# Kernel tuning notes

Measured on AMD Instinct MI355X. Metric: run time of the kernel, lower is better.

## Reference

```python
import jax, jax.numpy as jnp
import numpy as np

N = 100000   # nodes
E = 1000000  # edges per graph (avg degree 10)
D = 300      # feature dim


def _layernorm(x, gamma, beta, eps=1e-5):
    mu = jnp.mean(x, axis=-1, keepdims=True)
    var = jnp.mean(jnp.square(x - mu), axis=-1, keepdims=True)
    return (x - mu) * jax.lax.rsqrt(var + eps) * gamma + beta


def _graph_conv(edges, x, W, b, num_nodes):
    # DGL GraphConv with norm='both' and relu activation:
    # h = relu( D_in^{-1/2} A D_out^{-1/2} x W + b )
    src, dst = edges[0], edges[1]
    ones = jnp.ones((edges.shape[1],), x.dtype)
    out_deg = jax.ops.segment_sum(ones, src, num_segments=num_nodes)
    in_deg = jax.ops.segment_sum(ones, dst, num_segments=num_nodes)
    norm_src = jnp.where(out_deg > 0, jax.lax.rsqrt(jnp.maximum(out_deg, 1.0)), 0.0)
    norm_dst = jnp.where(in_deg > 0, jax.lax.rsqrt(jnp.maximum(in_deg, 1.0)), 0.0)
    h = x * norm_src[:, None]                                  # [N, D]
    agg = jax.ops.segment_sum(h[src], dst, num_segments=num_nodes)  # gather+scatter
    agg = agg * norm_dst[:, None]
    return jax.nn.relu(agg @ W + b)


def setup_inputs() -> dict:
    key = jax.random.key(0)
    ks = jax.random.split(key, 8)
    s = 0.05  # weight scale
    return {
        "table_feat": jax.random.normal(ks[0], (N, D), jnp.float32),
        "row_edges": jax.random.randint(ks[1], (2, E), 0, N, jnp.int32),
        "col_edges": jax.random.randint(ks[2], (2, E), 0, N, jnp.int32),
        "Wr": jax.random.normal(ks[3], (D, D), jnp.float32) * s,
        "br": jnp.zeros((D,), jnp.float32),
        "Wc": jax.random.normal(ks[4], (D, D), jnp.float32) * s,
        "bc": jnp.zeros((D,), jnp.float32),
        "Wrs": jax.random.normal(ks[5], (D, D), jnp.float32) * s,
        "brs": jnp.zeros((D,), jnp.float32),
        "g_rs": jnp.ones((D,), jnp.float32),
        "b_rs": jnp.zeros((D,), jnp.float32),
        "Wcs": jax.random.normal(ks[6], (D, D), jnp.float32) * s,
        "bcs": jnp.zeros((D,), jnp.float32),
        "g_cs": jnp.ones((D,), jnp.float32),
        "b_cs": jnp.zeros((D,), jnp.float32),
        "Wm": jax.random.normal(ks[7], (2 * D, D), jnp.float32) * s,
        "bm": jnp.zeros((D,), jnp.float32),
        "g_m": jnp.ones((D,), jnp.float32),
        "b_m": jnp.zeros((D,), jnp.float32),
    }


def reference(table_feat, row_edges, col_edges, Wr, br, Wc, bc,
              Wrs, brs, g_rs, b_rs, Wcs, bcs, g_cs, b_cs,
              Wm, bm, g_m, b_m):
    rowg = _graph_conv(row_edges, table_feat, Wr, br, N)   # row_aware GraphConv
    colg = _graph_conv(col_edges, table_feat, Wc, bc, N)   # col_aware GraphConv
    rowg = _layernorm(rowg @ Wrs + brs, g_rs, b_rs)        # row_graph_support
    colg = _layernorm(colg @ Wcs + bcs, g_cs, b_cs)        # col_graph_support
    merged = jnp.concatenate([rowg, colg], axis=1)          # [N, 2D]
    return _layernorm(merged @ Wm + bm, g_m, b_m)           # graph_merge
```

## Files before the change

kernel.cpp:

```cpp
#include <hip/hip_runtime.h>
#include <stdint.h>

#define SP 304
#define HSP 310
#define NT 10
#define KS300 19

typedef unsigned short u16;
using short8 = __attribute__((ext_vector_type(8))) short;
using f32x16 = __attribute__((ext_vector_type(16))) float;

__device__ __forceinline__ float b2f(u16 u) {
    return __uint_as_float(((unsigned)u) << 16);
}
__device__ __forceinline__ u16 f2b(float f) {
    unsigned u = __float_as_uint(f);
    return (u16)((u + 0x7FFFu + ((u >> 16) & 1u)) >> 16);
}
__device__ __forceinline__ float scrub(float v) {
    unsigned u = __float_as_uint(v);
    return (((u >> 23) & 0xFFu) == 0xFFu) ? 0.f : v;
}
__device__ __forceinline__ u16 sb16(u16 v) {
    return (((v >> 7) & 0xFFu) == 0xFFu) ? (u16)0 : v;
}

__global__ void detect_dtype(const u16* __restrict__ xs, int* __restrict__ flag) {
    __shared__ int cnt[256];
    int c = 0;
    for (int i = 0; i < 16; i++) {
        u16 v = xs[threadIdx.x * 16 + i];
        unsigned e = (v >> 7) & 0xFFu;
        c += (e >= 100u && e <= 150u) ? 1 : 0;
    }
    cnt[threadIdx.x] = c;
    __syncthreads();
    for (int s = 128; s > 0; s >>= 1) {
        if (threadIdx.x < s) cnt[threadIdx.x] += cnt[threadIdx.x + s];
        __syncthreads();
    }
    if (threadIdx.x == 0) flag[0] = (cnt[0] >= 3686) ? 1 : 0;
}

template<bool BF16>
__global__ __launch_bounds__(256) void conv_x(const void* __restrict__ x, u16* __restrict__ xb,
                                              int total4, const int* __restrict__ flag) {
    if ((flag[0] != 0) != BF16) return;
    int idx = blockIdx.x * 256 + threadIdx.x;
    if (idx >= total4) return;
    int node = idx / 76, c = idx - node * 76;
    ushort4 v = make_ushort4(0, 0, 0, 0);
    if (c < 75) {
        if (BF16) {
            v = *(const ushort4*)((const u16*)x + (size_t)node * 300 + c * 4);
            v.x = sb16(v.x); v.y = sb16(v.y); v.z = sb16(v.z); v.w = sb16(v.w);
        } else {
            float4 f = *(const float4*)((const float*)x + (size_t)node * 300 + c * 4);
            v = make_ushort4(f2b(scrub(f.x)), f2b(scrub(f.y)), f2b(scrub(f.z)), f2b(scrub(f.w)));
        }
    }
    *(ushort4*)(xb + (size_t)node * SP + c * 4) = v;
}

template<bool BF16>
__global__ void pack_b(const void* __restrict__ W, u16* __restrict__ P, int nseg,
                       const int* __restrict__ flag) {
    if ((flag[0] != 0) != BF16) return;
    int idx = blockIdx.x * 256 + threadIdx.x;
    int total = nseg * KS300 * NT * 512;
    if (idx >= total) return;
    int j = idx & 7, lane = (idx >> 3) & 63, t = idx >> 9;
    int nt = t % NT, ks = t / NT;
    int seg = ks / KS300, ksl = ks - seg * KS300;
    int kk = ksl * 16 + ((lane >> 5) << 3) + j;
    int n = nt * 32 + (lane & 31);
    u16 v = 0;
    if (kk < 300 && n < 300) {
        int wk = seg * 300 + kk;
        if (BF16) v = sb16(((const u16*)W)[(size_t)wk * 300 + n]);
        else      v = f2b(scrub(((const float*)W)[(size_t)wk * 300 + n]));
    }
    P[idx] = v;
}

template<bool BF16>
__global__ void conv_params(const void* p0, const void* p1, const void* p2, const void* p3,
                            const void* p4, const void* p5, const void* p6, const void* p7,
                            const void* p8, const void* p9, const void* p10,
                            float* __restrict__ pbuf, const int* __restrict__ flag) {
    if ((flag[0] != 0) != BF16) return;
    int idx = blockIdx.x * 256 + threadIdx.x;
    if (idx >= 11 * 304) return;
    int j = idx / 304, c = idx % 304;
    const void* ps[11] = {p0, p1, p2, p3, p4, p5, p6, p7, p8, p9, p10};
    float v = 0.f;
    if (c < 300) {
        if (BF16) v = b2f(sb16(((const u16*)ps[j])[c]));
        else      v = scrub(((const float*)ps[j])[c]);
    }
    pbuf[j * 304 + c] = v;
}

__global__ void count_deg(const int* __restrict__ src, const int* __restrict__ dst, int E,
                          int* __restrict__ outd, int* __restrict__ ind) {
    int e = blockIdx.x * 256 + threadIdx.x;
    if (e < E) {
        atomicAdd(&outd[src[e]], 1);
        atomicAdd(&ind[dst[e]], 1);
    }
}

__global__ __launch_bounds__(256) void alloc_norm(int Nn,
                           const int* __restrict__ odR, const int* __restrict__ idR,
                           const int* __restrict__ odC, const int* __restrict__ idC,
                           int* __restrict__ offR, int* __restrict__ offC,
                           float* __restrict__ nsR, float* __restrict__ ndR,
                           float* __restrict__ nsC, float* __restrict__ ndC,
                           int* __restrict__ cur2) {
    __shared__ int sR[256], sC[256];
    __shared__ int baseR, baseC;
    int tid = threadIdx.x;
    int i = blockIdx.x * 256 + tid;
    int dR = (i < Nn) ? idR[i] : 0;
    int dC = (i < Nn) ? idC[i] : 0;
    sR[tid] = dR; sC[tid] = dC;
    __syncthreads();
    for (int off = 1; off < 256; off <<= 1) {
        int vR = (tid >= off) ? sR[tid - off] : 0;
        int vC = (tid >= off) ? sC[tid - off] : 0;
        __syncthreads();
        sR[tid] += vR; sC[tid] += vC;
        __syncthreads();
    }
    if (tid == 0) {
        baseR = atomicAdd(&cur2[0], sR[255]);
        baseC = atomicAdd(&cur2[1], sC[255]);
    }
    __syncthreads();
    if (i < Nn) {
        offR[i] = baseR + sR[tid] - dR;
        offC[i] = baseC + sC[tid] - dC;
        nsR[i] = odR[i] > 0 ? rsqrtf((float)odR[i]) : 0.f;
        ndR[i] = idR[i] > 0 ? rsqrtf((float)idR[i]) : 0.f;
        nsC[i] = odC[i] > 0 ? rsqrtf((float)odC[i]) : 0.f;
        ndC[i] = idC[i] > 0 ? rsqrtf((float)idC[i]) : 0.f;
    }
}

__global__ void fill_csr(const int* __restrict__ src, const int* __restrict__ dst, int E,
                         const int* __restrict__ offs, int* __restrict__ cursor,
                         int* __restrict__ adj) {
    int e = blockIdx.x * 256 + threadIdx.x;
    if (e < E) {
        int d = dst[e];
        int p = offs[d] + atomicAdd(&cursor[d], 1);
        adj[p] = src[e];
    }
}

__global__ __launch_bounds__(256) void aggregate(
    const u16* __restrict__ xb, const int* __restrict__ adj, const int* __restrict__ offs,
    const int* __restrict__ deg, const float* __restrict__ ns, const float* __restrict__ nd,
    u16* __restrict__ agg, int Nn) {
    int w = threadIdx.x >> 6, lane = threadIdx.x & 63;
    int node = blockIdx.x * 4 + w;
    if (node >= Nn) return;
    int bg = offs[node], cnt = deg[node];
    const bool part = lane < 12;
    const int c0 = 4 * lane, c1 = 256 + 4 * lane;
    float a0 = 0, a1 = 0, a2 = 0, a3 = 0, p0 = 0, p1 = 0, p2 = 0, p3 = 0;
    int j = 0;
    for (; j + 4 <= cnt; j += 4) {
        int s0 = adj[bg + j], s1 = adj[bg + j + 1], s2 = adj[bg + j + 2], s3 = adj[bg + j + 3];
        float n0 = ns[s0], n1 = ns[s1], n2 = ns[s2], n3 = ns[s3];
        const u16* q0 = xb + (size_t)s0 * SP;
        const u16* q1 = xb + (size_t)s1 * SP;
        const u16* q2 = xb + (size_t)s2 * SP;
        const u16* q3 = xb + (size_t)s3 * SP;
        ushort4 v0 = *(const ushort4*)(q0 + c0);
        ushort4 v1 = *(const ushort4*)(q1 + c0);
        ushort4 v2 = *(const ushort4*)(q2 + c0);
        ushort4 v3 = *(const ushort4*)(q3 + c0);
        a0 += b2f(v0.x) * n0 + b2f(v1.x) * n1 + b2f(v2.x) * n2 + b2f(v3.x) * n3;
        a1 += b2f(v0.y) * n0 + b2f(v1.y) * n1 + b2f(v2.y) * n2 + b2f(v3.y) * n3;
        a2 += b2f(v0.z) * n0 + b2f(v1.z) * n1 + b2f(v2.z) * n2 + b2f(v3.z) * n3;
        a3 += b2f(v0.w) * n0 + b2f(v1.w) * n1 + b2f(v2.w) * n2 + b2f(v3.w) * n3;
        if (part) {
            ushort4 u0 = *(const ushort4*)(q0 + c1);
            ushort4 u1 = *(const ushort4*)(q1 + c1);
            ushort4 u2 = *(const ushort4*)(q2 + c1);
            ushort4 u3 = *(const ushort4*)(q3 + c1);
            p0 += b2f(u0.x) * n0 + b2f(u1.x) * n1 + b2f(u2.x) * n2 + b2f(u3.x) * n3;
            p1 += b2f(u0.y) * n0 + b2f(u1.y) * n1 + b2f(u2.y) * n2 + b2f(u3.y) * n3;
            p2 += b2f(u0.z) * n0 + b2f(u1.z) * n1 + b2f(u2.z) * n2 + b2f(u3.z) * n3;
            p3 += b2f(u0.w) * n0 + b2f(u1.w) * n1 + b2f(u2.w) * n2 + b2f(u3.w) * n3;
        }
    }
    for (; j < cnt; ++j) {
        int s = adj[bg + j];
        float nv = ns[s];
        const u16* rp = xb + (size_t)s * SP;
        ushort4 v = *(const ushort4*)(rp + c0);
        a0 += b2f(v.x) * nv; a1 += b2f(v.y) * nv; a2 += b2f(v.z) * nv; a3 += b2f(v.w) * nv;
        if (part) {
            ushort4 u = *(const ushort4*)(rp + c1);
            p0 += b2f(u.x) * nv; p1 += b2f(u.y) * nv; p2 += b2f(u.z) * nv; p3 += b2f(u.w) * nv;
        }
    }
    float ndv = nd[node];
    u16* o = agg + (size_t)node * SP;
    *(ushort4*)(o + c0) = make_ushort4(f2b(a0 * ndv), f2b(a1 * ndv), f2b(a2 * ndv), f2b(a3 * ndv));
    if (part)
        *(ushort4*)(o + c1) = make_ushort4(f2b(p0 * ndv), f2b(p1 * ndv), f2b(p2 * ndv), f2b(p3 * ndv));
}

__global__ __launch_bounds__(256, 3) void gemm_fused(
    const u16* __restrict__ Ain, const u16* __restrict__ B1p, const u16* __restrict__ B2p,
    const float* __restrict__ bias1, const float* __restrict__ bias2,
    const float* __restrict__ gamma2, const float* __restrict__ beta2,
    u16* __restrict__ outp, int M) {
    __shared__ __align__(16) char smem[2048 + 64 * HSP * 2];
    float* red = (float*)smem;
    u16* hb = (u16*)(smem + 2048);

    const int tid = threadIdx.x;
    const int w = tid >> 6, l = tid & 63;
    const int pr = w >> 1, sd = w & 1;
    const int mb = blockIdx.x * 64;
    const int r0 = mb + pr * 32;
    const bool act = r0 < M;
    const int lc = l & 31, hi = l >> 5;
    const int rowA = act ? min(r0 + lc, M - 1) : 0;
    const u16* a1 = Ain + (size_t)rowA * SP + hi * 8;
    const u16* bl1 = B1p + (size_t)(sd * 5) * 512 + (size_t)l * 8;
    const u16* bl2 = B2p + (size_t)(sd * 5) * 512 + (size_t)l * 8;
    const int colbase = sd * 160;

    f32x16 acc[5];
#pragma unroll
    for (int i = 0; i < 5; ++i)
#pragma unroll
        for (int r = 0; r < 16; ++r) acc[i][r] = 0.f;

    for (int ks = 0; ks < KS300; ++ks) {
        short8 af = *(const short8*)(a1 + ks * 16);
        const u16* bb = bl1 + (size_t)ks * (NT * 512);
#pragma unroll
        for (int i = 0; i < 5; ++i) {
            short8 bf = *(const short8*)(bb + i * 512);
            acc[i] = __builtin_amdgcn_mfma_f32_32x32x16_bf16(af, bf, acc[i], 0, 0, 0);
        }
    }
    if (act) {
#pragma unroll
        for (int i = 0; i < 5; ++i) {
            int col = colbase + i * 32 + lc;
            if (col < 304) {
                float bb = col < 300 ? bias1[col] : 0.f;
#pragma unroll
                for (int r = 0; r < 16; ++r) {
                    int rowl = 4 * hi + (r & 3) + 8 * (r >> 2);
                    float v = scrub(acc[i][r] + bb);
                    v = v > 0.f ? v : 0.f;
                    hb[(size_t)(pr * 32 + rowl) * HSP + col] = col < 300 ? f2b(v) : (u16)0;
                }
            }
        }
    }
    __syncthreads();

#pragma unroll
    for (int i = 0; i < 5; ++i)
#pragma unroll
        for (int r = 0; r < 16; ++r) acc[i][r] = 0.f;
    const u16* hrow = hb + (size_t)(pr * 32 + lc) * HSP + hi * 8;
    for (int ks = 0; ks < KS300; ++ks) {
        short8 af = *(const short8*)(hrow + ks * 16);
        const u16* bb = bl2 + (size_t)ks * (NT * 512);
#pragma unroll
        for (int i = 0; i < 5; ++i) {
            short8 bf = *(const short8*)(bb + i * 512);
            acc[i] = __builtin_amdgcn_mfma_f32_32x32x16_bf16(af, bf, acc[i], 0, 0, 0);
        }
    }

    float sum[16], ssq[16];
#pragma unroll
    for (int r = 0; r < 16; ++r) { sum[r] = 0.f; ssq[r] = 0.f; }
#pragma unroll
    for (int i = 0; i < 5; ++i) {
        int col = colbase + i * 32 + lc;
        bool cv = col < 300;
        float bb = cv ? bias2[col] : 0.f;
#pragma unroll
        for (int r = 0; r < 16; ++r) {
            float v = cv ? scrub(acc[i][r] + bb) : 0.f;
            acc[i][r] = v;
            sum[r] += v;
            ssq[r] += v * v;
        }
    }
#pragma unroll
    for (int off = 1; off < 32; off <<= 1) {
#pragma unroll
        for (int r = 0; r < 16; ++r) {
            sum[r] += __shfl_xor(sum[r], off);
            ssq[r] += __shfl_xor(ssq[r], off);
        }
    }
    if (act) {
#pragma unroll
        for (int r = 0; r < 16; ++r) {
            if (lc == r) {
                int rowl = 4 * hi + (r & 3) + 8 * (r >> 2);
                float* q = red + ((pr * 2 + sd) * 32 + rowl) * 2;
                q[0] = sum[r]; q[1] = ssq[r];
            }
        }
    }
    __syncthreads();
    float mean[16], inv[16];
    if (act) {
#pragma unroll
        for (int r = 0; r < 16; ++r) {
            int rowl = 4 * hi + (r & 3) + 8 * (r >> 2);
            const float* q = red + ((pr * 2 + (1 - sd)) * 32 + rowl) * 2;
            float s = sum[r] + q[0], qq = ssq[r] + q[1];
            mean[r] = s * (1.f / 300.f);
            float var = fmaxf(qq * (1.f / 300.f) - mean[r] * mean[r], 0.f);
            inv[r] = rsqrtf(var + 1e-5f);
        }
    }

    u16* stg = hb;
    if (act) {
#pragma unroll
        for (int i = 0; i < 5; ++i) {
            int col = colbase + i * 32 + lc;
            if (col < 304) {
                float g = col < 300 ? gamma2[col] : 0.f;
                float be = col < 300 ? beta2[col] : 0.f;
#pragma unroll
                for (int r = 0; r < 16; ++r) {
                    int rowl = 4 * hi + (r & 3) + 8 * (r >> 2);
                    float v = (acc[i][r] - mean[r]) * inv[r] * g + be;
                    stg[(size_t)(pr * 32 + rowl) * SP + col] = col < 300 ? f2b(v) : (u16)0;
                }
            }
        }
    }
    __syncthreads();
    int rows = min(64, M - mb);
    u16* dst = outp + (size_t)mb * SP;
    if (rows == 64) {
#pragma unroll
        for (int k = 0; k < 10; ++k) {
            int idx = k * 256 + tid;
            if (idx < 2432) *(short8*)(dst + idx * 8) = *(const short8*)(stg + idx * 8);
        }
    } else {
        for (int idx = tid; idx < rows * SP; idx += 256) dst[idx] = stg[idx];
    }
}

template<int MODE, bool OUTF32>
__global__ __launch_bounds__(256, 3) void gemm_f(
    const u16* __restrict__ A1, const u16* __restrict__ A2,
    const u16* __restrict__ Bp, const float* __restrict__ bias,
    const float* __restrict__ gamma, const float* __restrict__ beta,
    void* __restrict__ out, int M, const int* __restrict__ flag) {
    if (MODE == 2) {
        if ((flag[0] != 0) != (!OUTF32)) return;
    }
    __shared__ __align__(16) char smem[2048 + 38912];
    float* red = (float*)smem;

    const int tid = threadIdx.x;
    const int w = tid >> 6, l = tid & 63;
    const int pr = w >> 1, sd = w & 1;
    const int mb = blockIdx.x * 64;
    const int r0 = mb + pr * 32;
    const bool act = r0 < M;
    const int lc = l & 31, hi = l >> 5;
    const int rowA = act ? min(r0 + lc, M - 1) : 0;
    const u16* a1 = A1 + (size_t)rowA * SP + hi * 8;
    const u16* a2 = A2 + (size_t)rowA * SP + hi * 8;
    const u16* bl = Bp + (size_t)(sd * 5) * 512 + (size_t)l * 8;
    const int colbase = sd * 160;

    f32x16 acc[5];
#pragma unroll
    for (int i = 0; i < 5; ++i)
#pragma unroll
        for (int r = 0; r < 16; ++r) acc[i][r] = 0.f;

    for (int ks = 0; ks < KS300; ++ks) {
        short8 af = *(const short8*)(a1 + ks * 16);
        const u16* bb = bl + (size_t)ks * (NT * 512);
#pragma unroll
        for (int i = 0; i < 5; ++i) {
            short8 bf = *(const short8*)(bb + i * 512);
            acc[i] = __builtin_amdgcn_mfma_f32_32x32x16_bf16(af, bf, acc[i], 0, 0, 0);
        }
    }
    if (MODE == 2) {
        for (int ks = KS300; ks < 2 * KS300; ++ks) {
            short8 af = *(const short8*)(a2 + (ks - KS300) * 16);
            const u16* bb = bl + (size_t)ks * (NT * 512);
#pragma unroll
            for (int i = 0; i < 5; ++i) {
                short8 bf = *(const short8*)(bb + i * 512);
                acc[i] = __builtin_amdgcn_mfma_f32_32x32x16_bf16(af, bf, acc[i], 0, 0, 0);
            }
        }
    }

    float sum[16], ssq[16];
#pragma unroll
    for (int r = 0; r < 16; ++r) { sum[r] = 0.f; ssq[r] = 0.f; }
#pragma unroll
    for (int i = 0; i < 5; ++i) {
        int col = colbase + i * 32 + lc;
        bool cv = col < 300;
        float bb = cv ? bias[col] : 0.f;
#pragma unroll
        for (int r = 0; r < 16; ++r) {
            float v = cv ? scrub(acc[i][r] + bb) : 0.f;
            acc[i][r] = v;
            sum[r] += v;
            ssq[r] += v * v;
        }
    }
#pragma unroll
    for (int off = 1; off < 32; off <<= 1) {
#pragma unroll
        for (int r = 0; r < 16; ++r) {
            sum[r] += __shfl_xor(sum[r], off);
            ssq[r] += __shfl_xor(ssq[r], off);
        }
    }
    if (act) {
#pragma unroll
        for (int r = 0; r < 16; ++r) {
            if (lc == r) {
                int rowl = 4 * hi + (r & 3) + 8 * (r >> 2);
                float* q = red + ((pr * 2 + sd) * 32 + rowl) * 2;
                q[0] = sum[r]; q[1] = ssq[r];
            }
        }
    }
    __syncthreads();
    float mean[16], inv[16];
    if (act) {
#pragma unroll
        for (int r = 0; r < 16; ++r) {
            int rowl = 4 * hi + (r & 3) + 8 * (r >> 2);
            const float* q = red + ((pr * 2 + (1 - sd)) * 32 + rowl) * 2;
            float s = sum[r] + q[0], qq = ssq[r] + q[1];
            mean[r] = s * (1.f / 300.f);
            float var = fmaxf(qq * (1.f / 300.f) - mean[r] * mean[r], 0.f);
            inv[r] = rsqrtf(var + 1e-5f);
        }
    }

    if (!OUTF32) {
        u16* stg = (u16*)(smem + 2048);
        if (act) {
#pragma unroll
            for (int i = 0; i < 5; ++i) {
                int col = colbase + i * 32 + lc;
                if (col < 300) {
                    float g = gamma[col], be = beta[col];
#pragma unroll
                    for (int r = 0; r < 16; ++r) {
                        int rowl = 4 * hi + (r & 3) + 8 * (r >> 2);
                        float v = (acc[i][r] - mean[r]) * inv[r] * g + be;
                        stg[(pr * 32 + rowl) * 300 + col] = f2b(v);
                    }
                }
            }
        }
        __syncthreads();
        int rows = min(64, M - mb);
        u16* dst = (u16*)out + (size_t)mb * 300;
        if (rows == 64) {
#pragma unroll
            for (int k = 0; k < 10; ++k) {
                int idx = k * 256 + tid;
                if (idx < 2400) *(short8*)(dst + idx * 8) = *(const short8*)(stg + idx * 8);
            }
        } else {
            for (int idx = tid; idx < rows * 300; idx += 256) dst[idx] = stg[idx];
        }
    } else {
        float* fst = (float*)(smem + 2048);
        for (int pp = 0; pp < 2; ++pp) {
            __syncthreads();
            if (pr == pp && act) {
#pragma unroll
                for (int i = 0; i < 5; ++i) {
                    int col = colbase + i * 32 + lc;
                    if (col < 300) {
                        float g = gamma[col], be = beta[col];
#pragma unroll
                        for (int r = 0; r < 16; ++r) {
                            int rowl = 4 * hi + (r & 3) + 8 * (r >> 2);
                            float v = (acc[i][r] - mean[r]) * inv[r] * g + be;
                            fst[rowl * 300 + col] = v;
                        }
                    }
                }
            }
            __syncthreads();
            int tr0 = mb + pp * 32;
            if (tr0 < M) {
                int rows = min(32, M - tr0);
                float* dst = (float*)out + (size_t)tr0 * 300;
                if (rows == 32) {
#pragma unroll
                    for (int k = 0; k < 10; ++k) {
                        int idx = k * 256 + tid;
                        if (idx < 2400) *(float4*)(dst + idx * 4) = *(const float4*)(fst + idx * 4);
                    }
                } else {
                    for (int idx = tid; idx < rows * 300; idx += 256) dst[idx] = fst[idx];
                }
            }
        }
    }
}

extern "C" void kernel_launch(void* const* d_in, const int* in_sizes, int n_in,
                              void* d_out, int out_size, void* d_ws, size_t ws_size,
                              hipStream_t stream) {
    (void)n_in; (void)out_size; (void)ws_size;
    const void* x   = d_in[0];
    const int* re   = (const int*)d_in[1];
    const int* ce   = (const int*)d_in[2];

    const int Nn = in_sizes[0] / 300;
    const int Er = in_sizes[1] / 2;
    const int Ec = in_sizes[2] / 2;

    char* p = (char*)d_ws;
    size_t off = 0;
    auto balloc = [&](size_t bytes) -> void* {
        void* r = p + off;
        off += (bytes + 255) & ~(size_t)255;
        return r;
    };
    int* degR  = (int*)balloc((size_t)Nn * 4);
    int* odegR = (int*)balloc((size_t)Nn * 4);
    int* degC  = (int*)balloc((size_t)Nn * 4);
    int* odegC = (int*)balloc((size_t)Nn * 4);
    int* curR  = (int*)balloc((size_t)Nn * 4);
    int* curC  = (int*)balloc((size_t)Nn * 4);
    int* cur2  = (int*)balloc(64 * 4);
    size_t zbytes = off;
    int* flag  = (int*)balloc(256);
    int* offsR = (int*)balloc((size_t)Nn * 4);
    int* offsC = (int*)balloc((size_t)Nn * 4);
    float* nsR = (float*)balloc((size_t)Nn * 4);
    float* ndR = (float*)balloc((size_t)Nn * 4);
    float* nsC = (float*)balloc((size_t)Nn * 4);
    float* ndC = (float*)balloc((size_t)Nn * 4);
    int* adjR  = (int*)balloc((size_t)Er * 4);
    int* adjC  = (int*)balloc((size_t)Ec * 4);
    const size_t PB1 = (size_t)KS300 * NT * 512;
    u16* WrP   = (u16*)balloc(PB1 * 2);
    u16* WcP   = (u16*)balloc(PB1 * 2);
    u16* WrsP  = (u16*)balloc(PB1 * 2);
    u16* WcsP  = (u16*)balloc(PB1 * 2);
    u16* WmP   = (u16*)balloc(2 * PB1 * 2);
    float* pbuf = (float*)balloc(11 * 304 * 4);
    u16* xb    = (u16*)balloc((size_t)Nn * SP * 2);
    u16* B2    = (u16*)balloc((size_t)Nn * SP * 2);
    u16* B3    = (u16*)balloc((size_t)Nn * SP * 2);

    const float* pbr  = pbuf + 0 * 304;
    const float* pbc  = pbuf + 1 * 304;
    const float* pbrs = pbuf + 2 * 304;
    const float* pgrs = pbuf + 3 * 304;
    const float* pBrs = pbuf + 4 * 304;
    const float* pbcs = pbuf + 5 * 304;
    const float* pgcs = pbuf + 6 * 304;
    const float* pBcs = pbuf + 7 * 304;
    const float* pbm  = pbuf + 8 * 304;
    const float* pgm  = pbuf + 9 * 304;
    const float* pBm  = pbuf + 10 * 304;

    detect_dtype<<<1, 256, 0, stream>>>((const u16*)x, flag);
    hipMemsetAsync(d_ws, 0, zbytes, stream);

    const int total4 = Nn * 76;
    conv_x<true><<<(total4 + 255) / 256, 256, 0, stream>>>(x, xb, total4, flag);
    conv_x<false><<<(total4 + 255) / 256, 256, 0, stream>>>(x, xb, total4, flag);

#define PK(Wsrc, Pdst, nseg)                                                                  \
    pack_b<true><<<(int)(((nseg) * PB1 + 255) / 256), 256, 0, stream>>>(Wsrc, Pdst, nseg, flag); \
    pack_b<false><<<(int)(((nseg) * PB1 + 255) / 256), 256, 0, stream>>>(Wsrc, Pdst, nseg, flag)
    PK(d_in[3], WrP, 1);
    PK(d_in[5], WcP, 1);
    PK(d_in[7], WrsP, 1);
    PK(d_in[11], WcsP, 1);
    PK(d_in[15], WmP, 2);
#undef PK

    conv_params<true><<<14, 256, 0, stream>>>(d_in[4], d_in[6], d_in[8], d_in[9], d_in[10],
                                              d_in[12], d_in[13], d_in[14], d_in[16], d_in[17],
                                              d_in[18], pbuf, flag);
    conv_params<false><<<14, 256, 0, stream>>>(d_in[4], d_in[6], d_in[8], d_in[9], d_in[10],
                                               d_in[12], d_in[13], d_in[14], d_in[16], d_in[17],
                                               d_in[18], pbuf, flag);

    count_deg<<<(Er + 255) / 256, 256, 0, stream>>>(re, re + Er, Er, odegR, degR);
    count_deg<<<(Ec + 255) / 256, 256, 0, stream>>>(ce, ce + Ec, Ec, odegC, degC);
    alloc_norm<<<(Nn + 255) / 256, 256, 0, stream>>>(Nn, odegR, degR, odegC, degC,
                                                     offsR, offsC, nsR, ndR, nsC, ndC, cur2);
    fill_csr<<<(Er + 255) / 256, 256, 0, stream>>>(re, re + Er, Er, offsR, curR, adjR);
    fill_csr<<<(Ec + 255) / 256, 256, 0, stream>>>(ce, ce + Ec, Ec, offsC, curC, adjC);

    aggregate<<<(Nn + 3) / 4, 256, 0, stream>>>(xb, adjR, offsR, degR, nsR, ndR, B2, Nn);
    aggregate<<<(Nn + 3) / 4, 256, 0, stream>>>(xb, adjC, offsC, degC, nsC, ndC, B3, Nn);

    const int gb = (Nn + 63) / 64;
    gemm_fused<<<gb, 256, 0, stream>>>(B2, WrP, WrsP, pbr, pbrs, pgrs, pBrs, B2, Nn);
    gemm_fused<<<gb, 256, 0, stream>>>(B3, WcP, WcsP, pbc, pbcs, pgcs, pBcs, B3, Nn);
    gemm_f<2, false><<<gb, 256, 0, stream>>>(B2, B3, WmP, pbm, pgm, pBm, d_out, Nn, flag);
    gemm_f<2, true ><<<gb, 256, 0, stream>>>(B2, B3, WmP, pbm, pgm, pBm, d_out, Nn, flag);
}
```

Before: 1.127 ms.

## Stage GEMM A tiles through LDS and merge dtype-templated kernel launches

The GEMM kernels now copy each 64-row A tile into shared memory with coalesced 16-byte loads before the MFMA loops, instead of each lane reading its A fragments straight from global memory. The same LDS buffer is reused for the hidden activations and for the output staging, with added barriers between phases. Separately, the paired true/false template launches for dtype conversion, weight packing, parameter conversion and the merge GEMM become single kernels that branch on the runtime flag. This halves the launch count for those stages, at the cost of extra synchronisation and a runtime dtype branch.

```diff
diff --git a/kernel.cpp b/kernel.cpp
--- a/kernel.cpp
+++ b/kernel.cpp
@@ -2,7 +2,7 @@
 #include <stdint.h>
 
 #define SP 304
-#define HSP 310
+#define ASP 312
 #define NT 10
 #define KS300 19
 
@@ -42,10 +42,9 @@
     if (threadIdx.x == 0) flag[0] = (cnt[0] >= 3686) ? 1 : 0;
 }
 
-template<bool BF16>
 __global__ __launch_bounds__(256) void conv_x(const void* __restrict__ x, u16* __restrict__ xb,
                                               int total4, const int* __restrict__ flag) {
-    if ((flag[0] != 0) != BF16) return;
+    const bool BF16 = flag[0] != 0;
     int idx = blockIdx.x * 256 + threadIdx.x;
     if (idx >= total4) return;
     int node = idx / 76, c = idx - node * 76;
@@ -62,10 +61,9 @@
     *(ushort4*)(xb + (size_t)node * SP + c * 4) = v;
 }
 
-template<bool BF16>
 __global__ void pack_b(const void* __restrict__ W, u16* __restrict__ P, int nseg,
                        const int* __restrict__ flag) {
-    if ((flag[0] != 0) != BF16) return;
+    const bool BF16 = flag[0] != 0;
     int idx = blockIdx.x * 256 + threadIdx.x;
     int total = nseg * KS300 * NT * 512;
     if (idx >= total) return;
@@ -83,12 +81,11 @@
     P[idx] = v;
 }
 
-template<bool BF16>
 __global__ void conv_params(const void* p0, const void* p1, const void* p2, const void* p3,
                             const void* p4, const void* p5, const void* p6, const void* p7,
                             const void* p8, const void* p9, const void* p10,
                             float* __restrict__ pbuf, const int* __restrict__ flag) {
-    if ((flag[0] != 0) != BF16) return;
+    const bool BF16 = flag[0] != 0;
     int idx = blockIdx.x * 256 + threadIdx.x;
     if (idx >= 11 * 304) return;
     int j = idx / 304, c = idx % 304;
@@ -214,12 +211,21 @@
         *(ushort4*)(o + c1) = make_ushort4(f2b(p0 * ndv), f2b(p1 * ndv), f2b(p2 * ndv), f2b(p3 * ndv));
 }
 
+__device__ __forceinline__ void stage_a(const u16* __restrict__ A, u16* __restrict__ lds,
+                                        int mb, int M, int tid) {
+    for (int idx = tid; idx < 64 * 38; idx += 256) {
+        int row = idx / 38, ck = idx - row * 38;
+        int gr = min(mb + row, M - 1);
+        *(short8*)(lds + row * ASP + ck * 8) = *(const short8*)(A + (size_t)gr * SP + ck * 8);
+    }
+}
+
 __global__ __launch_bounds__(256, 3) void gemm_fused(
     const u16* __restrict__ Ain, const u16* __restrict__ B1p, const u16* __restrict__ B2p,
     const float* __restrict__ bias1, const float* __restrict__ bias2,
     const float* __restrict__ gamma2, const float* __restrict__ beta2,
     u16* __restrict__ outp, int M) {
-    __shared__ __align__(16) char smem[2048 + 64 * HSP * 2];
+    __shared__ __align__(16) char smem[2048 + 64 * ASP * 2];
     float* red = (float*)smem;
     u16* hb = (u16*)(smem + 2048);
 
@@ -230,11 +236,13 @@
     const int r0 = mb + pr * 32;
     const bool act = r0 < M;
     const int lc = l & 31, hi = l >> 5;
-    const int rowA = act ? min(r0 + lc, M - 1) : 0;
-    const u16* a1 = Ain + (size_t)rowA * SP + hi * 8;
     const u16* bl1 = B1p + (size_t)(sd * 5) * 512 + (size_t)l * 8;
     const u16* bl2 = B2p + (size_t)(sd * 5) * 512 + (size_t)l * 8;
     const int colbase = sd * 160;
+    const u16* arow = hb + (size_t)(pr * 32 + lc) * ASP + hi * 8;
+
+    stage_a(Ain, hb, mb, M, tid);
+    __syncthreads();
 
     f32x16 acc[5];
 #pragma unroll
@@ -243,7 +251,7 @@
         for (int r = 0; r < 16; ++r) acc[i][r] = 0.f;
 
     for (int ks = 0; ks < KS300; ++ks) {
-        short8 af = *(const short8*)(a1 + ks * 16);
+        short8 af = *(const short8*)(arow + ks * 16);
         const u16* bb = bl1 + (size_t)ks * (NT * 512);
 #pragma unroll
         for (int i = 0; i < 5; ++i) {
@@ -251,6 +259,8 @@
             acc[i] = __builtin_amdgcn_mfma_f32_32x32x16_bf16(af, bf, acc[i], 0, 0, 0);
         }
     }
+    __syncthreads();
+
     if (act) {
 #pragma unroll
         for (int i = 0; i < 5; ++i) {
@@ -262,7 +272,7 @@
                     int rowl = 4 * hi + (r & 3) + 8 * (r >> 2);
                     float v = scrub(acc[i][r] + bb);
                     v = v > 0.f ? v : 0.f;
-                    hb[(size_t)(pr * 32 + rowl) * HSP + col] = col < 300 ? f2b(v) : (u16)0;
+                    hb[(size_t)(pr * 32 + rowl) * ASP + col] = col < 300 ? f2b(v) : (u16)0;
                 }
             }
         }
@@ -273,9 +283,8 @@
     for (int i = 0; i < 5; ++i)
 #pragma unroll
         for (int r = 0; r < 16; ++r) acc[i][r] = 0.f;
-    const u16* hrow = hb + (size_t)(pr * 32 + lc) * HSP + hi * 8;
     for (int ks = 0; ks < KS300; ++ks) {
-        short8 af = *(const short8*)(hrow + ks * 16);
+        short8 af = *(const short8*)(arow + ks * 16);
         const u16* bb = bl2 + (size_t)ks * (NT * 512);
 #pragma unroll
         for (int i = 0; i < 5; ++i) {
@@ -363,17 +372,15 @@
     }
 }
 
-template<int MODE, bool OUTF32>
-__global__ __launch_bounds__(256, 3) void gemm_f(
+__global__ __launch_bounds__(256, 3) void gemm_merge(
     const u16* __restrict__ A1, const u16* __restrict__ A2,
     const u16* __restrict__ Bp, const float* __restrict__ bias,
     const float* __restrict__ gamma, const float* __restrict__ beta,
     void* __restrict__ out, int M, const int* __restrict__ flag) {
-    if (MODE == 2) {
-        if ((flag[0] != 0) != (!OUTF32)) return;
-    }
-    __shared__ __align__(16) char smem[2048 + 38912];
+    const bool f32out = (flag[0] == 0);
+    __shared__ __align__(16) char smem[2048 + 64 * ASP * 2];
     float* red = (float*)smem;
+    u16* hb = (u16*)(smem + 2048);
 
     const int tid = threadIdx.x;
     const int w = tid >> 6, l = tid & 63;
@@ -382,11 +389,9 @@
     const int r0 = mb + pr * 32;
     const bool act = r0 < M;
     const int lc = l & 31, hi = l >> 5;
-    const int rowA = act ? min(r0 + lc, M - 1) : 0;
-    const u16* a1 = A1 + (size_t)rowA * SP + hi * 8;
-    const u16* a2 = A2 + (size_t)rowA * SP + hi * 8;
     const u16* bl = Bp + (size_t)(sd * 5) * 512 + (size_t)l * 8;
     const int colbase = sd * 160;
+    const u16* arow = hb + (size_t)(pr * 32 + lc) * ASP + hi * 8;
 
     f32x16 acc[5];
 #pragma unroll
@@ -394,8 +399,10 @@
 #pragma unroll
         for (int r = 0; r < 16; ++r) acc[i][r] = 0.f;
 
+    stage_a(A1, hb, mb, M, tid);
+    __syncthreads();
     for (int ks = 0; ks < KS300; ++ks) {
-        short8 af = *(const short8*)(a1 + ks * 16);
+        short8 af = *(const short8*)(arow + ks * 16);
         const u16* bb = bl + (size_t)ks * (NT * 512);
 #pragma unroll
         for (int i = 0; i < 5; ++i) {
@@ -403,15 +410,16 @@
             acc[i] = __builtin_amdgcn_mfma_f32_32x32x16_bf16(af, bf, acc[i], 0, 0, 0);
         }
     }
-    if (MODE == 2) {
-        for (int ks = KS300; ks < 2 * KS300; ++ks) {
-            short8 af = *(const short8*)(a2 + (ks - KS300) * 16);
-            const u16* bb = bl + (size_t)ks * (NT * 512);
-#pragma unroll
-            for (int i = 0; i < 5; ++i) {
-                short8 bf = *(const short8*)(bb + i * 512);
-                acc[i] = __builtin_amdgcn_mfma_f32_32x32x16_bf16(af, bf, acc[i], 0, 0, 0);
-            }
+    __syncthreads();
+    stage_a(A2, hb, mb, M, tid);
+    __syncthreads();
+    for (int ks = KS300; ks < 2 * KS300; ++ks) {
+        short8 af = *(const short8*)(arow + (ks - KS300) * 16);
+        const u16* bb = bl + (size_t)ks * (NT * 512);
+#pragma unroll
+        for (int i = 0; i < 5; ++i) {
+            short8 bf = *(const short8*)(bb + i * 512);
+            acc[i] = __builtin_amdgcn_mfma_f32_32x32x16_bf16(af, bf, acc[i], 0, 0, 0);
         }
     }
 
@@ -463,8 +471,8 @@
         }
     }
 
-    if (!OUTF32) {
-        u16* stg = (u16*)(smem + 2048);
+    if (!f32out) {
+        u16* stg = hb;
         if (act) {
 #pragma unroll
             for (int i = 0; i < 5; ++i) {
@@ -493,7 +501,7 @@
             for (int idx = tid; idx < rows * 300; idx += 256) dst[idx] = stg[idx];
         }
     } else {
-        float* fst = (float*)(smem + 2048);
+        float* fst = (float*)hb;
         for (int pp = 0; pp < 2; ++pp) {
             __syncthreads();
             if (pr == pp && act) {
@@ -593,12 +601,10 @@
     hipMemsetAsync(d_ws, 0, zbytes, stream);
 
     const int total4 = Nn * 76;
-    conv_x<true><<<(total4 + 255) / 256, 256, 0, stream>>>(x, xb, total4, flag);
-    conv_x<false><<<(total4 + 255) / 256, 256, 0, stream>>>(x, xb, total4, flag);
+    conv_x<<<(total4 + 255) / 256, 256, 0, stream>>>(x, xb, total4, flag);
 
 #define PK(Wsrc, Pdst, nseg)                                                                  \
-    pack_b<true><<<(int)(((nseg) * PB1 + 255) / 256), 256, 0, stream>>>(Wsrc, Pdst, nseg, flag); \
-    pack_b<false><<<(int)(((nseg) * PB1 + 255) / 256), 256, 0, stream>>>(Wsrc, Pdst, nseg, flag)
+    pack_b<<<(int)(((nseg) * PB1 + 255) / 256), 256, 0, stream>>>(Wsrc, Pdst, nseg, flag)
     PK(d_in[3], WrP, 1);
     PK(d_in[5], WcP, 1);
     PK(d_in[7], WrsP, 1);
@@ -606,12 +612,9 @@
     PK(d_in[15], WmP, 2);
 #undef PK
 
-    conv_params<true><<<14, 256, 0, stream>>>(d_in[4], d_in[6], d_in[8], d_in[9], d_in[10],
-                                              d_in[12], d_in[13], d_in[14], d_in[16], d_in[17],
-                                              d_in[18], pbuf, flag);
-    conv_params<false><<<14, 256, 0, stream>>>(d_in[4], d_in[6], d_in[8], d_in[9], d_in[10],
-                                               d_in[12], d_in[13], d_in[14], d_in[16], d_in[17],
-                                               d_in[18], pbuf, flag);
+    conv_params<<<14, 256, 0, stream>>>(d_in[4], d_in[6], d_in[8], d_in[9], d_in[10],
+                                        d_in[12], d_in[13], d_in[14], d_in[16], d_in[17],
+                                        d_in[18], pbuf, flag);
 
     count_deg<<<(Er + 255) / 256, 256, 0, stream>>>(re, re + Er, Er, odegR, degR);
     count_deg<<<(Ec + 255) / 256, 256, 0, stream>>>(ce, ce + Ec, Ec, odegC, degC);
@@ -626,6 +629,5 @@
     const int gb = (Nn + 63) / 64;
     gemm_fused<<<gb, 256, 0, stream>>>(B2, WrP, WrsP, pbr, pbrs, pgrs, pBrs, B2, Nn);
     gemm_fused<<<gb, 256, 0, stream>>>(B3, WcP, WcsP, pbc, pbcs, pgcs, pBcs, B3, Nn);
-    gemm_f<2, false><<<gb, 256, 0, stream>>>(B2, B3, WmP, pbm, pgm, pBm, d_out, Nn, flag);
-    gemm_f<2, true ><<<gb, 256, 0, stream>>>(B2, B3, WmP, pbm, pgm, pBm, d_out, Nn, flag);
-}
+    gemm_merge<<<gb, 256, 0, stream>>>(B2, B3, WmP, pbm, pgm, pBm, d_out, Nn, flag);
+}
```

Measured after the change: 1.121 ms. No clear change (-0.5%).
